# Optimization experiments

Measured on AMD Instinct MI355X. Metric: run time of the kernel, lower is better.

## Reference

```python
import jax, jax.numpy as jnp
import numpy as np

NUM_NODES = 100000
NUM_EDGES = 1600000
IN_DIM, HID_DIM, OUT_DIM = 128, 128, 70


def gcn_conv(x, edge_index, W, b):
    """PyG-style GCNConv: linear transform, add self-loops, symmetric
    degree-normalized scatter-add aggregation, plus bias."""
    n = x.shape[0]
    xw = x @ W  # [N, D_out]
    src, dst = edge_index[0], edge_index[1]  # messages flow src -> dst
    loop = jnp.arange(n)
    src = jnp.concatenate([src, loop])
    dst = jnp.concatenate([dst, loop])
    # degree computed at target nodes (with self-loops), edge weight 1
    deg = jax.ops.segment_sum(jnp.ones_like(dst, dtype=xw.dtype), dst,
                              num_segments=n)
    dinv = jnp.where(deg > 0, jax.lax.rsqrt(deg), 0.0)
    norm = dinv[src] * dinv[dst]  # [E+N]
    msgs = xw[src] * norm[:, None]  # [E+N, D_out] gathered messages
    out = jax.ops.segment_sum(msgs, dst, num_segments=n)
    return out + b


def setup_inputs() -> dict:
    key = jax.random.key(0)
    k = jax.random.split(key, 6)
    x = jax.random.normal(k[0], (NUM_NODES, IN_DIM), dtype=jnp.float32)
    edge_index = jax.random.randint(k[1], (2, NUM_EDGES), 0, NUM_NODES,
                                    dtype=jnp.int64)
    # Glorot-style init for weights, zero bias (PyG default)
    W1 = jax.random.normal(k[2], (IN_DIM, HID_DIM), dtype=jnp.float32) / np.sqrt(IN_DIM)
    b1 = jnp.zeros((HID_DIM,), dtype=jnp.float32)
    W2 = jax.random.normal(k[3], (HID_DIM, OUT_DIM), dtype=jnp.float32) / np.sqrt(HID_DIM)
    b2 = jnp.zeros((OUT_DIM,), dtype=jnp.float32)
    return {"x": x, "edge_index": edge_index, "W1": W1, "b1": b1,
            "W2": W2, "b2": b2}


def reference(x, edge_index, W1, b1, W2, b2):
    h = gcn_conv(x, edge_index, W1, b1)
    h = jax.nn.relu(h)
    # dropout(p=0.5) is identity in eval mode
    out = gcn_conv(h, edge_index, W2, b2)
    return out
```

## Files before the change

kernel.cpp:

```cpp
#include <hip/hip_runtime.h>
#include <hip/hip_bf16.h>


#define BSH 8
#define BCHUNK 8192

typedef __attribute__((ext_vector_type(8))) short short8;
typedef __attribute__((ext_vector_type(4))) float float4v;
typedef __attribute__((ext_vector_type(2))) float float2v;

__device__ __forceinline__ float bf_lo(unsigned u) { return __uint_as_float(u << 16); }
__device__ __forceinline__ float bf_hi(unsigned u) { return __uint_as_float(u & 0xffff0000u); }
__device__ __forceinline__ float bf2f(unsigned short h) {
    return __uint_as_float((unsigned)h << 16);
}
__device__ __forceinline__ unsigned short f2bf(float f) {
    unsigned u = __float_as_uint(f);
    u += 0x7fff + ((u >> 16) & 1);
    return (unsigned short)(u >> 16);
}
__device__ __forceinline__ void acc8(float* acc, uint4 m) {
    acc[0] += bf_lo(m.x); acc[1] += bf_hi(m.x);
    acc[2] += bf_lo(m.y); acc[3] += bf_hi(m.y);
    acc[4] += bf_lo(m.z); acc[5] += bf_hi(m.z);
    acc[6] += bf_lo(m.w); acc[7] += bf_hi(m.w);
}


__global__ void k_bucket_hist(const int* __restrict__ dst, int* __restrict__ bhist,
                              int E, int nb) {
    __shared__ int h[512];
    int t = threadIdx.x;
    for (int j = t; j < nb; j += blockDim.x) h[j] = 0;
    __syncthreads();
    int i = blockIdx.x * blockDim.x + t;
    int stride = gridDim.x * blockDim.x;
    for (; i < E; i += stride) atomicAdd(&h[dst[i] >> BSH], 1);
    __syncthreads();
    for (int j = t; j < nb; j += blockDim.x) {
        int c = h[j];
        if (c) atomicAdd(&bhist[j], c);
    }
}

__global__ void k_bucket_scan(const int* __restrict__ bhist, int* __restrict__ bbase,
                              int* __restrict__ bwcur, int nb, int E) {
    __shared__ int s[512];
    int t = threadIdx.x;
    int v = (t < nb) ? bhist[t] : 0;
    s[t] = v;
    __syncthreads();
    for (int off = 1; off < 512; off <<= 1) {
        int add = (t >= off) ? s[t - off] : 0;
        __syncthreads();
        s[t] += add;
        __syncthreads();
    }
    if (t < nb) {
        int excl = s[t] - v;
        bbase[t] = excl;
        bwcur[t] = excl;
    }
    if (t == 0) bbase[nb] = E;
}

__global__ void k_bucket_scatter(const int* __restrict__ src, const int* __restrict__ dst,
                                 int* __restrict__ bwcur,
                                 unsigned long long* __restrict__ tmp, int E, int nb) {
    __shared__ int lh[512];
    __shared__ int lb[512];
    int t = threadIdx.x;
    for (int j = t; j < nb; j += 256) lh[j] = 0;
    __syncthreads();
    int e0 = blockIdx.x * BCHUNK;
    int e1 = min(E, e0 + BCHUNK);
    for (int e = e0 + t; e < e1; e += 256) atomicAdd(&lh[dst[e] >> BSH], 1);
    __syncthreads();
    for (int j = t; j < nb; j += 256) {
        int c = lh[j];
        lb[j] = c ? atomicAdd(&bwcur[j], c) : 0;
        lh[j] = 0;
    }
    __syncthreads();
    for (int e = e0 + t; e < e1; e += 256) {
        int d = dst[e];
        int b = d >> BSH;
        int o = atomicAdd(&lh[b], 1);
        tmp[lb[b] + o] = ((unsigned long long)(unsigned)d << 32) | (unsigned)src[e];
    }
}

__global__ void k_bucket_finalize(const unsigned long long* __restrict__ tmp,
                                  const int* __restrict__ bbase,
                                  int* __restrict__ deg, float* __restrict__ dinv,
                                  int* __restrict__ rs, int* __restrict__ csr, int N) {
    __shared__ int cnt[256];
    __shared__ int sc[256];
    int b = blockIdx.x;
    int t = threadIdx.x;
    int e0 = bbase[b], e1 = bbase[b + 1];
    cnt[t] = 0;
    __syncthreads();
    for (int e = e0 + t; e < e1; e += 256) {
        int d = (int)(tmp[e] >> 32);
        atomicAdd(&cnt[d & 255], 1);
    }
    __syncthreads();
    int c = cnt[t];
    sc[t] = c;
    __syncthreads();
    for (int off = 1; off < 256; off <<= 1) {
        int add = (t >= off) ? sc[t - off] : 0;
        __syncthreads();
        sc[t] += add;
        __syncthreads();
    }
    int excl = sc[t] - c;
    __syncthreads();
    sc[t] = excl;
    int node = (b << BSH) + t;
    if (node < N) {
        deg[node] = c;
        dinv[node] = rsqrtf((float)(c + 1));
        rs[node] = e0 + excl;
    }
    cnt[t] = 0;
    __syncthreads();
    for (int e = e0 + t; e < e1; e += 256) {
        unsigned long long p = tmp[e];
        int j = ((int)(p >> 32)) & 255;
        int o = atomicAdd(&cnt[j], 1);
        csr[e0 + sc[j] + o] = (int)(p & 0xffffffffu);
    }
}

__global__ void k_prep_w(const float* __restrict__ W, unsigned short* __restrict__ Wth,
                         unsigned short* __restrict__ Wtl, int DOUT, int COLS) {
    int i = blockIdx.x * blockDim.x + threadIdx.x;
    if (i >= COLS * 128) return;
    int col = i % COLS;
    int k = i / COLS;
    float w = (col < DOUT) ? W[k * DOUT + col] : 0.f;
    unsigned short h = f2bf(w);
    Wth[(size_t)col * 128 + k] = h;
    Wtl[(size_t)col * 128 + k] = f2bf(w - bf2f(h));
}

template <int DOUT, int OSTRIDE, int NT>
__global__ __launch_bounds__(256, 3) void k_gemm_mfma(
        const float* __restrict__ X, const unsigned short* __restrict__ Wth,
        const unsigned short* __restrict__ Wtl,
        const float* __restrict__ dinv, unsigned short* __restrict__ Y, int n) {
    __shared__ short xs_h[64][136];
    __shared__ short xs_l[64][136];
    int t = threadIdx.x;
    int lane = t & 63, wave = t >> 6;
    int m16 = lane & 15, quad = lane >> 4;
    int r0 = blockIdx.x * 64;

    short8 bh[2][4], bl[2][4];
    int nt0 = wave, nt1 = wave + 4;
#pragma unroll
    for (int i = 0; i < 2; i++) {
        int nt = i ? nt1 : nt0;
        if (nt >= NT) continue;
        int col = nt * 16 + m16;
#pragma unroll
        for (int kc = 0; kc < 4; kc++) {
            bh[i][kc] = *(const short8*)&Wth[(size_t)col * 128 + kc * 32 + quad * 8];
            bl[i][kc] = *(const short8*)&Wtl[(size_t)col * 128 + kc * 32 + quad * 8];
        }
    }

    for (int p = t; p < 64 * 64; p += 256) {
        int row = p >> 6;
        int kk = p & 63;
        int gr = r0 + row;
        if (gr >= n) gr = n - 1;
        float2v xv = __builtin_nontemporal_load(
            (const float2v*)(X + (size_t)gr * 128 + 2 * kk));
        unsigned short h0 = f2bf(xv.x), h1 = f2bf(xv.y);
        unsigned short l0 = f2bf(xv.x - bf2f(h0)), l1 = f2bf(xv.y - bf2f(h1));
        *(unsigned*)&xs_h[row][2 * kk] = (unsigned)h0 | ((unsigned)h1 << 16);
        *(unsigned*)&xs_l[row][2 * kk] = (unsigned)l0 | ((unsigned)l1 << 16);
    }
    __syncthreads();

    float4v acc[2][4];
#pragma unroll
    for (int i = 0; i < 2; i++)
#pragma unroll
        for (int ms = 0; ms < 4; ms++) acc[i][ms] = (float4v){0.f, 0.f, 0.f, 0.f};

#pragma unroll
    for (int kc = 0; kc < 4; kc++) {
#pragma unroll
        for (int ms = 0; ms < 4; ms++) {
            short8 ah = *(short8*)&xs_h[ms * 16 + m16][kc * 32 + quad * 8];
            short8 al = *(short8*)&xs_l[ms * 16 + m16][kc * 32 + quad * 8];
#pragma unroll
            for (int i = 0; i < 2; i++) {
                int nt = i ? nt1 : nt0;
                if (nt >= NT) continue;
                acc[i][ms] = __builtin_amdgcn_mfma_f32_16x16x32_bf16(ah, bh[i][kc], acc[i][ms], 0, 0, 0);
                acc[i][ms] = __builtin_amdgcn_mfma_f32_16x16x32_bf16(al, bh[i][kc], acc[i][ms], 0, 0, 0);
                acc[i][ms] = __builtin_amdgcn_mfma_f32_16x16x32_bf16(ah, bl[i][kc], acc[i][ms], 0, 0, 0);
            }
        }
    }

#pragma unroll
    for (int i = 0; i < 2; i++) {
        int nt = i ? nt1 : nt0;
        if (nt >= NT) continue;
        int col = nt * 16 + m16;
        if (col >= OSTRIDE) continue;
#pragma unroll
        for (int ms = 0; ms < 4; ms++) {
#pragma unroll
            for (int r = 0; r < 4; r++) {
                int row = r0 + ms * 16 + quad * 4 + r;
                if (row < n) {
                    float val = (col < DOUT) ? acc[i][ms][r] * dinv[row] : 0.f;
                    Y[(size_t)row * OSTRIDE + col] = f2bf(val);
                }
            }
        }
    }
}

__global__ __launch_bounds__(256, 8) void k_agg_w128(
        const uint4* __restrict__ msg, const float* __restrict__ dinv,
        const int* __restrict__ rs, const int* __restrict__ deg,
        const int* __restrict__ csr, const float* __restrict__ bias,
        float* __restrict__ out, int n) {
    int lane = threadIdx.x & 63;
    int q = lane & 15;
    int slot = lane >> 4;
    int wid = blockIdx.x * 4 + (threadIdx.x >> 6);
    int nw = gridDim.x * 4;
    for (int v = wid; v < n; v += nw) {
        int start = rs[v];
        int cnt = deg[v];
        float dv = dinv[v];
        uint4 mself = msg[(size_t)v * 16 + q];
        float acc[8] = {0.f, 0.f, 0.f, 0.f, 0.f, 0.f, 0.f, 0.f};
        int i = slot;
        for (; i + 4 < cnt; i += 8) {
            int s0 = csr[start + i];
            int s1 = csr[start + i + 4];
            uint4 m0 = msg[(size_t)s0 * 16 + q];
            uint4 m1 = msg[(size_t)s1 * 16 + q];
            acc8(acc, m0);
            acc8(acc, m1);
        }
        if (i < cnt) {
            int s = csr[start + i];
            uint4 m = msg[(size_t)s * 16 + q];
            acc8(acc, m);
        }
#pragma unroll
        for (int j = 0; j < 8; j++) acc[j] += __shfl_xor(acc[j], 32);
#pragma unroll
        for (int j = 0; j < 8; j++) acc[j] += __shfl_xor(acc[j], 16);
        if (slot == 0) {
            float o[8];
            o[0] = acc[0] + bf_lo(mself.x); o[1] = acc[1] + bf_hi(mself.x);
            o[2] = acc[2] + bf_lo(mself.y); o[3] = acc[3] + bf_hi(mself.y);
            o[4] = acc[4] + bf_lo(mself.z); o[5] = acc[5] + bf_hi(mself.z);
            o[6] = acc[6] + bf_lo(mself.w); o[7] = acc[7] + bf_hi(mself.w);
            float r[8];
#pragma unroll
            for (int j = 0; j < 8; j++) r[j] = fmaxf(dv * o[j] + bias[8 * q + j], 0.f);
            float4v* op = (float4v*)(out + (size_t)v * 128 + 8 * q);
            __builtin_nontemporal_store((float4v){r[0], r[1], r[2], r[3]}, op);
            __builtin_nontemporal_store((float4v){r[4], r[5], r[6], r[7]}, op + 1);
        }
    }
}

__global__ __launch_bounds__(256, 8) void k_agg_w72(
        const uint4* __restrict__ msg, const float* __restrict__ dinv,
        const int* __restrict__ rs, const int* __restrict__ deg,
        const int* __restrict__ csr, const float* __restrict__ bias,
        float* __restrict__ out, int n) {
    int lane = threadIdx.x & 63;
    int slot = lane / 9;
    int q = lane - slot * 9;
    bool active = lane < 63;
    int wid = blockIdx.x * 4 + (threadIdx.x >> 6);
    int nw = gridDim.x * 4;
    for (int v = wid; v < n; v += nw) {
        int start = rs[v];
        int cnt = deg[v];
        float dv = dinv[v];
        float acc[8] = {0.f, 0.f, 0.f, 0.f, 0.f, 0.f, 0.f, 0.f};
        uint4 mself = make_uint4(0, 0, 0, 0);
        if (active) {
            mself = msg[(size_t)v * 9 + q];
            int i = slot;
            for (; i + 7 < cnt; i += 14) {
                int s0 = csr[start + i];
                int s1 = csr[start + i + 7];
                uint4 m0 = msg[(size_t)s0 * 9 + q];
                uint4 m1 = msg[(size_t)s1 * 9 + q];
                acc8(acc, m0);
                acc8(acc, m1);
            }
            if (i < cnt) {
                int s = csr[start + i];
                uint4 m = msg[(size_t)s * 9 + q];
                acc8(acc, m);
            }
        }
#pragma unroll
        for (int j = 0; j < 8; j++) {
            float t27 = __shfl(acc[j], lane + 27);
            if (lane < 27) acc[j] += t27;
        }
#pragma unroll
        for (int j = 0; j < 8; j++) {
            float t54 = __shfl(acc[j], lane + 54);
            float t9  = __shfl(acc[j], lane + 9);
            float t18 = __shfl(acc[j], lane + 18);
            if (lane < 9) acc[j] += t54 + t9 + t18;
        }
        if (lane < 9) {
            float o[8];
            o[0] = acc[0] + bf_lo(mself.x); o[1] = acc[1] + bf_hi(mself.x);
            o[2] = acc[2] + bf_lo(mself.y); o[3] = acc[3] + bf_hi(mself.y);
            o[4] = acc[4] + bf_lo(mself.z); o[5] = acc[5] + bf_hi(mself.z);
            o[6] = acc[6] + bf_lo(mself.w); o[7] = acc[7] + bf_hi(mself.w);
            float* orow = out + (size_t)v * 70 + 8 * q;
#pragma unroll
            for (int jj = 0; jj < 4; jj++) {
                int f = 8 * q + 2 * jj;
                if (f < 70) {
                    float2v st = {dv * o[2 * jj] + bias[f],
                                  dv * o[2 * jj + 1] + bias[f + 1]};
                    __builtin_nontemporal_store(st, (float2v*)(orow + 2 * jj));
                }
            }
        }
    }
}

static inline size_t alignup(size_t x) { return (x + 255) & ~(size_t)255; }

extern "C" void kernel_launch(void* const* d_in, const int* in_sizes, int n_in,
                              void* d_out, int out_size, void* d_ws, size_t ws_size,
                              hipStream_t stream) {
    const float* x = (const float*)d_in[0];
    const int* edge = (const int*)d_in[1];
    const float* W1 = (const float*)d_in[2];
    const float* b1 = (const float*)d_in[3];
    const float* W2 = (const float*)d_in[4];
    const float* b2 = (const float*)d_in[5];

    const int N = in_sizes[0] / 128;
    const int E = in_sizes[1] / 2;
    const int* src = edge;
    const int* dst = edge + E;
    const int nb = (N + 255) >> BSH;

    char* w = (char*)d_ws;
    int* deg = (int*)w;              w += alignup((size_t)N * 4);
    float* dinv = (float*)w;         w += alignup((size_t)N * 4);
    int* rs = (int*)w;               w += alignup((size_t)N * 4);
    int* bhist = (int*)w;            w += alignup(4096);
    int* bbase = (int*)w;            w += alignup(4096);
    int* bwcur = (int*)w;            w += alignup(4096);
    int* csr = (int*)w;              w += alignup((size_t)E * 4);
    unsigned short* msg1 = (unsigned short*)w; w += alignup((size_t)N * 128 * 2);
    unsigned short* msg2 = (unsigned short*)w; w += alignup((size_t)N * 72 * 2);
    unsigned short* w1th = (unsigned short*)w; w += alignup(128 * 128 * 2);
    unsigned short* w1tl = (unsigned short*)w; w += alignup(128 * 128 * 2);
    unsigned short* w2th = (unsigned short*)w; w += alignup(80 * 128 * 2);
    unsigned short* w2tl = (unsigned short*)w; w += alignup(80 * 128 * 2);
    float* h = (float*)w;            w += alignup((size_t)N * 128 * 4);
    unsigned long long* tmp = (unsigned long long*)h;

    k_prep_w<<<(128 * 128 + 255) / 256, 256, 0, stream>>>(W1, w1th, w1tl, 128, 128);
    k_prep_w<<<(80 * 128 + 255) / 256, 256, 0, stream>>>(W2, w2th, w2tl, 70, 80);

    hipMemsetAsync(bhist, 0, (size_t)(nb + 1) * 4, stream);
    k_bucket_hist<<<256, 256, 0, stream>>>(dst, bhist, E, nb);
    k_bucket_scan<<<1, 512, 0, stream>>>(bhist, bbase, bwcur, nb, E);
    k_bucket_scatter<<<(E + BCHUNK - 1) / BCHUNK, 256, 0, stream>>>(src, dst, bwcur, tmp, E, nb);
    k_bucket_finalize<<<nb, 256, 0, stream>>>(tmp, bbase, deg, dinv, rs, csr, N);

    int gblocks = (N + 63) / 64;

    k_gemm_mfma<128, 128, 8><<<gblocks, 256, 0, stream>>>(x, w1th, w1tl, dinv, msg1, N);
    k_agg_w128<<<2048, 256, 0, stream>>>((const uint4*)msg1, dinv, rs, deg, csr, b1, h, N);

    k_gemm_mfma<70, 72, 5><<<gblocks, 256, 0, stream>>>(h, w2th, w2tl, dinv, msg2, N);
    k_agg_w72<<<2048, 256, 0, stream>>>((const uint4*)msg2, dinv, rs, deg, csr, b2,
                                        (float*)d_out, N);
}
```

Before: 393.1 us.

## Store messages in 16-column chunk-major layout and aggregate per chunk

The GEMM now writes its bf16 messages in a chunk-major layout of 16 columns per chunk, so each chunk table is a small contiguous array. Both aggregation kernels are replaced by one templated kernel in which each block group handles a single chunk and each pair of lanes aggregates one node over all of its edges serially. The goal is to shrink the gathered working set per block group so it stays in L2/MALL and to remove the cross-lane shuffle reductions. In exchange, the CSR indices are re-read once per chunk, per-lane edge loops are divergent, and each gather is only 32 bytes, which wastes cache-line bandwidth.

```diff
diff --git a/kernel.cpp b/kernel.cpp
--- a/kernel.cpp
+++ b/kernel.cpp
@@ -146,7 +146,7 @@
     Wtl[(size_t)col * 128 + k] = f2bf(w - bf2f(h));
 }
 
-template <int DOUT, int OSTRIDE, int NT>
+template <int DOUT, int NCOLS, int NT>
 __global__ __launch_bounds__(256, 3) void k_gemm_mfma(
         const float* __restrict__ X, const unsigned short* __restrict__ Wth,
         const unsigned short* __restrict__ Wtl,
@@ -214,7 +214,7 @@
         int nt = i ? nt1 : nt0;
         if (nt >= NT) continue;
         int col = nt * 16 + m16;
-        if (col >= OSTRIDE) continue;
+        if (col >= NCOLS) continue;
 #pragma unroll
         for (int ms = 0; ms < 4; ms++) {
 #pragma unroll
@@ -222,123 +222,89 @@
                 int row = r0 + ms * 16 + quad * 4 + r;
                 if (row < n) {
                     float val = (col < DOUT) ? acc[i][ms][r] * dinv[row] : 0.f;
-                    Y[(size_t)row * OSTRIDE + col] = f2bf(val);
+                    Y[((size_t)nt * n + row) * 16 + m16] = f2bf(val);
                 }
             }
         }
     }
 }
 
-__global__ __launch_bounds__(256, 8) void k_agg_w128(
+template <int NCH, bool RELU, int DOUT, int OSTRIDE>
+__global__ __launch_bounds__(256, 8) void k_agg_chunk(
         const uint4* __restrict__ msg, const float* __restrict__ dinv,
         const int* __restrict__ rs, const int* __restrict__ deg,
         const int* __restrict__ csr, const float* __restrict__ bias,
         float* __restrict__ out, int n) {
+    int k = blockIdx.x & 7;
+    int c, iw, ng;
+    if (NCH == 8) {
+        c = k; iw = 0; ng = 1;
+    } else {
+        const int cm[8] = {0, 0, 1, 1, 2, 3, 3, 4};
+        const int im[8] = {0, 1, 0, 1, 0, 0, 1, 0};
+        const int nbk[5] = {2, 2, 1, 2, 1};
+        c = cm[k]; iw = im[k]; ng = nbk[c];
+    }
+    int bpg = gridDim.x >> 3;
+    int wid = (iw * bpg + (blockIdx.x >> 3)) * 4 + (threadIdx.x >> 6);
+    int nw = ng * bpg * 4;
     int lane = threadIdx.x & 63;
-    int q = lane & 15;
-    int slot = lane >> 4;
-    int wid = blockIdx.x * 4 + (threadIdx.x >> 6);
-    int nw = gridDim.x * 4;
-    for (int v = wid; v < n; v += nw) {
-        int start = rs[v];
-        int cnt = deg[v];
-        float dv = dinv[v];
-        uint4 mself = msg[(size_t)v * 16 + q];
+    int pr = lane >> 1;
+    int q = lane & 1;
+    const uint4* mc = msg + (size_t)c * n * 2;
+    for (int base = wid * 32; base < n; base += nw * 32) {
+        int v = base + pr;
+        bool valid = v < n;
+        int start = 0, cnt = 0;
+        float dv = 0.f;
+        if (valid) { start = rs[v]; cnt = deg[v]; dv = dinv[v]; }
         float acc[8] = {0.f, 0.f, 0.f, 0.f, 0.f, 0.f, 0.f, 0.f};
-        int i = slot;
-        for (; i + 4 < cnt; i += 8) {
+        int i = 0;
+        for (; i + 3 < cnt; i += 4) {
             int s0 = csr[start + i];
-            int s1 = csr[start + i + 4];
-            uint4 m0 = msg[(size_t)s0 * 16 + q];
-            uint4 m1 = msg[(size_t)s1 * 16 + q];
+            int s1 = csr[start + i + 1];
+            int s2 = csr[start + i + 2];
+            int s3 = csr[start + i + 3];
+            uint4 m0 = mc[(size_t)s0 * 2 + q];
+            uint4 m1 = mc[(size_t)s1 * 2 + q];
+            uint4 m2 = mc[(size_t)s2 * 2 + q];
+            uint4 m3 = mc[(size_t)s3 * 2 + q];
             acc8(acc, m0);
             acc8(acc, m1);
-        }
-        if (i < cnt) {
-            int s = csr[start + i];
-            uint4 m = msg[(size_t)s * 16 + q];
+            acc8(acc, m2);
+            acc8(acc, m3);
+        }
+        for (; i < cnt; i++) {
+            uint4 m = mc[(size_t)csr[start + i] * 2 + q];
             acc8(acc, m);
         }
-#pragma unroll
-        for (int j = 0; j < 8; j++) acc[j] += __shfl_xor(acc[j], 32);
-#pragma unroll
-        for (int j = 0; j < 8; j++) acc[j] += __shfl_xor(acc[j], 16);
-        if (slot == 0) {
+        if (valid) {
+            uint4 ms = mc[(size_t)v * 2 + q];
             float o[8];
-            o[0] = acc[0] + bf_lo(mself.x); o[1] = acc[1] + bf_hi(mself.x);
-            o[2] = acc[2] + bf_lo(mself.y); o[3] = acc[3] + bf_hi(mself.y);
-            o[4] = acc[4] + bf_lo(mself.z); o[5] = acc[5] + bf_hi(mself.z);
-            o[6] = acc[6] + bf_lo(mself.w); o[7] = acc[7] + bf_hi(mself.w);
+            o[0] = acc[0] + bf_lo(ms.x); o[1] = acc[1] + bf_hi(ms.x);
+            o[2] = acc[2] + bf_lo(ms.y); o[3] = acc[3] + bf_hi(ms.y);
+            o[4] = acc[4] + bf_lo(ms.z); o[5] = acc[5] + bf_hi(ms.z);
+            o[6] = acc[6] + bf_lo(ms.w); o[7] = acc[7] + bf_hi(ms.w);
+            int f0 = c * 16 + 8 * q;
             float r[8];
 #pragma unroll
-            for (int j = 0; j < 8; j++) r[j] = fmaxf(dv * o[j] + bias[8 * q + j], 0.f);
-            float4v* op = (float4v*)(out + (size_t)v * 128 + 8 * q);
-            __builtin_nontemporal_store((float4v){r[0], r[1], r[2], r[3]}, op);
-            __builtin_nontemporal_store((float4v){r[4], r[5], r[6], r[7]}, op + 1);
-        }
-    }
-}
-
-__global__ __launch_bounds__(256, 8) void k_agg_w72(
-        const uint4* __restrict__ msg, const float* __restrict__ dinv,
-        const int* __restrict__ rs, const int* __restrict__ deg,
-        const int* __restrict__ csr, const float* __restrict__ bias,
-        float* __restrict__ out, int n) {
-    int lane = threadIdx.x & 63;
-    int slot = lane / 9;
-    int q = lane - slot * 9;
-    bool active = lane < 63;
-    int wid = blockIdx.x * 4 + (threadIdx.x >> 6);
-    int nw = gridDim.x * 4;
-    for (int v = wid; v < n; v += nw) {
-        int start = rs[v];
-        int cnt = deg[v];
-        float dv = dinv[v];
-        float acc[8] = {0.f, 0.f, 0.f, 0.f, 0.f, 0.f, 0.f, 0.f};
-        uint4 mself = make_uint4(0, 0, 0, 0);
-        if (active) {
-            mself = msg[(size_t)v * 9 + q];
-            int i = slot;
-            for (; i + 7 < cnt; i += 14) {
-                int s0 = csr[start + i];
-                int s1 = csr[start + i + 7];
-                uint4 m0 = msg[(size_t)s0 * 9 + q];
-                uint4 m1 = msg[(size_t)s1 * 9 + q];
-                acc8(acc, m0);
-                acc8(acc, m1);
+            for (int j = 0; j < 8; j++) {
+                float b = (f0 + j < DOUT) ? bias[f0 + j] : 0.f;
+                float val = dv * o[j] + b;
+                r[j] = RELU ? fmaxf(val, 0.f) : val;
             }
-            if (i < cnt) {
-                int s = csr[start + i];
-                uint4 m = msg[(size_t)s * 9 + q];
-                acc8(acc, m);
-            }
-        }
-#pragma unroll
-        for (int j = 0; j < 8; j++) {
-            float t27 = __shfl(acc[j], lane + 27);
-            if (lane < 27) acc[j] += t27;
-        }
-#pragma unroll
-        for (int j = 0; j < 8; j++) {
-            float t54 = __shfl(acc[j], lane + 54);
-            float t9  = __shfl(acc[j], lane + 9);
-            float t18 = __shfl(acc[j], lane + 18);
-            if (lane < 9) acc[j] += t54 + t9 + t18;
-        }
-        if (lane < 9) {
-            float o[8];
-            o[0] = acc[0] + bf_lo(mself.x); o[1] = acc[1] + bf_hi(mself.x);
-            o[2] = acc[2] + bf_lo(mself.y); o[3] = acc[3] + bf_hi(mself.y);
-            o[4] = acc[4] + bf_lo(mself.z); o[5] = acc[5] + bf_hi(mself.z);
-            o[6] = acc[6] + bf_lo(mself.w); o[7] = acc[7] + bf_hi(mself.w);
-            float* orow = out + (size_t)v * 70 + 8 * q;
-#pragma unroll
-            for (int jj = 0; jj < 4; jj++) {
-                int f = 8 * q + 2 * jj;
-                if (f < 70) {
-                    float2v st = {dv * o[2 * jj] + bias[f],
-                                  dv * o[2 * jj + 1] + bias[f + 1]};
-                    __builtin_nontemporal_store(st, (float2v*)(orow + 2 * jj));
+            if (OSTRIDE == 128) {
+                float4v* op = (float4v*)(out + (size_t)v * OSTRIDE + f0);
+                __builtin_nontemporal_store((float4v){r[0], r[1], r[2], r[3]}, op);
+                __builtin_nontemporal_store((float4v){r[4], r[5], r[6], r[7]}, op + 1);
+            } else {
+#pragma unroll
+                for (int jj = 0; jj < 4; jj++) {
+                    int f = f0 + 2 * jj;
+                    if (f < DOUT) {
+                        float2 st = make_float2(r[2 * jj], r[2 * jj + 1]);
+                        *(float2*)(out + (size_t)v * OSTRIDE + f) = st;
+                    }
                 }
             }
         }
@@ -372,7 +338,7 @@
     int* bwcur = (int*)w;            w += alignup(4096);
     int* csr = (int*)w;              w += alignup((size_t)E * 4);
     unsigned short* msg1 = (unsigned short*)w; w += alignup((size_t)N * 128 * 2);
-    unsigned short* msg2 = (unsigned short*)w; w += alignup((size_t)N * 72 * 2);
+    unsigned short* msg2 = (unsigned short*)w; w += alignup((size_t)N * 80 * 2);
     unsigned short* w1th = (unsigned short*)w; w += alignup(128 * 128 * 2);
     unsigned short* w1tl = (unsigned short*)w; w += alignup(128 * 128 * 2);
     unsigned short* w2th = (unsigned short*)w; w += alignup(80 * 128 * 2);
@@ -392,9 +358,10 @@
     int gblocks = (N + 63) / 64;
 
     k_gemm_mfma<128, 128, 8><<<gblocks, 256, 0, stream>>>(x, w1th, w1tl, dinv, msg1, N);
-    k_agg_w128<<<2048, 256, 0, stream>>>((const uint4*)msg1, dinv, rs, deg, csr, b1, h, N);
-
-    k_gemm_mfma<70, 72, 5><<<gblocks, 256, 0, stream>>>(h, w2th, w2tl, dinv, msg2, N);
-    k_agg_w72<<<2048, 256, 0, stream>>>((const uint4*)msg2, dinv, rs, deg, csr, b2,
-                                        (float*)d_out, N);
-}
+    k_agg_chunk<8, true, 128, 128><<<2048, 256, 0, stream>>>(
+        (const uint4*)msg1, dinv, rs, deg, csr, b1, h, N);
+
+    k_gemm_mfma<70, 80, 5><<<gblocks, 256, 0, stream>>>(h, w2th, w2tl, dinv, msg2, N);
+    k_agg_chunk<5, false, 70, 70><<<2048, 256, 0, stream>>>(
+        (const uint4*)msg2, dinv, rs, deg, csr, b2, (float*)d_out, N);
+}
```

Result: slower. 454.5 us (+15.6%).
